# Optimization experiments

Measured on AMD Instinct MI355X. Metric: run time of the kernel, lower is better.

## Reference

```python
import jax, jax.numpy as jnp
import numpy as np
import math

N = 50000        # nodes
E = 800000       # edges
FEATS = 64
CLASSES = 16
HIDDEN = 64
DEPTH = 10
DIFF = 0.9
EMB_DIM = 1 + int(math.log2(FEATS))   # 7
ADJ_HID = 4 + EMB_DIM                  # 11


def setup_inputs() -> dict:
    key = jax.random.key(0)
    ks = jax.random.split(key, 12)
    x = jax.random.normal(ks[0], (N, FEATS), dtype=jnp.float32)
    src = jax.random.randint(ks[1], (E,), 0, N, dtype=jnp.int64)
    dst = jax.random.randint(ks[2], (E,), 0, N, dtype=jnp.int64)
    s = 0.05
    W1 = jax.random.normal(ks[3], (2 * FEATS, HIDDEN), jnp.float32) * s
    b1 = jnp.zeros((HIDDEN,), jnp.float32)
    W2 = jax.random.normal(ks[4], (HIDDEN, CLASSES), jnp.float32) * s
    b2 = jnp.zeros((CLASSES,), jnp.float32)
    A1 = jax.random.normal(ks[5], (2 + EMB_DIM, ADJ_HID), jnp.float32) * s
    ab1 = jnp.zeros((ADJ_HID,), jnp.float32)
    A2 = jax.random.normal(ks[6], (ADJ_HID, 1), jnp.float32) * s
    ab2 = jnp.zeros((1,), jnp.float32)
    emb = jax.random.normal(ks[7], (FEATS, EMB_DIM), jnp.float32) * s
    return {"x": x, "src": src, "dst": dst, "W1": W1, "b1": b1,
            "W2": W2, "b2": b2, "A1": A1, "ab1": ab1, "A2": A2,
            "ab2": ab2, "emb": emb}


def reference(x, src, dst, W1, b1, W2, b2, A1, ab1, A2, ab2, emb):
    n, f = x.shape
    # cached symmetric GCN normalization: D^-1/2 A D^-1/2
    deg = jax.ops.segment_sum(jnp.ones((src.shape[0],), x.dtype), dst, num_segments=n)
    inv_sqrt = jnp.where(deg > 0, jax.lax.rsqrt(jnp.maximum(deg, 1e-12)), 0.0)
    norm = inv_sqrt[src] * inv_sqrt[dst]   # [E]

    def conv(z):
        return jax.ops.segment_sum(z[src] * norm[:, None], dst, num_segments=n)

    # first diffusion loop (personalized-pagerank style residual blend)
    h0 = x
    z = x
    for _ in range(DEPTH):
        z = conv(z) * DIFF + (1.0 - DIFF) * h0

    # node x class pair MLP (class-major flatten, matching x.t().reshape(-1,1))
    cls = jnp.repeat(jnp.arange(f), n)                 # [f*n]
    pairs = jnp.concatenate([z.T.reshape(-1, 1),
                             h0.T.reshape(-1, 1),
                             emb[cls]], axis=1)        # [f*n, 2+EMB_DIM]
    u = jax.nn.relu(pairs @ A1 + ab1)
    u = (u @ A2 + ab2) / 2.0                           # [f*n, 1]
    z = u.reshape(f, n).T                              # [n, f]

    # dropout is identity in eval mode
    z = jnp.concatenate([z, h0], axis=1)               # [n, 2f]
    z = jax.nn.relu(z @ W1 + b1)
    z = z @ W2 + b2                                    # [n, classes]

    # second diffusion loop over class logits
    g0 = z
    for _ in range(DEPTH):
        z = conv(z) * DIFF + (1.0 - DIFF) * g0
    return z
```

## Files before the change

### kernel.cpp

```cpp
#include <hip/hip_runtime.h>

#define FEATS    64
#define CLASSES  16
#define EMB_DIM  7
#define ADJ_HID  11
#define DIFF     0.9f

__device__ inline float bf2f(unsigned short u) {
    return __uint_as_float(((unsigned int)u) << 16);
}
__device__ inline unsigned short f2bf(float f) {
    unsigned int u = __float_as_uint(f);
    return (unsigned short)((u + 0x7FFFu + ((u >> 16) & 1u)) >> 16);
}


__global__ __launch_bounds__(256) void k_deg(const int* __restrict__ dst, int* __restrict__ deg, int e) {
    int i = blockIdx.x * 256 + threadIdx.x;
    if (i < e) atomicAdd(&deg[dst[i]], 1);
}

__global__ __launch_bounds__(256) void k_invs(const int* __restrict__ deg, float* __restrict__ invs, int n) {
    int i = blockIdx.x * 256 + threadIdx.x;
    if (i < n) { int d = deg[i]; invs[i] = d > 0 ? rsqrtf((float)d) : 0.f; }
}

__global__ __launch_bounds__(256) void k_scan1(const int* __restrict__ deg, int* __restrict__ rowptr,
                                               int* __restrict__ bsum, int n) {
    __shared__ int s[256];
    int tid = threadIdx.x;
    int i = blockIdx.x * 256 + tid;
    int v = (i < n) ? deg[i] : 0;
    s[tid] = v; __syncthreads();
    for (int ofs = 1; ofs < 256; ofs <<= 1) {
        int t = (tid >= ofs) ? s[tid - ofs] : 0;
        __syncthreads(); s[tid] += t; __syncthreads();
    }
    if (i < n) rowptr[i] = s[tid] - v;
    if (tid == 255) bsum[blockIdx.x] = s[255];
}

__global__ __launch_bounds__(256) void k_scan2(int* __restrict__ bsum, int nb) {
    __shared__ int s[256];
    int tid = threadIdx.x;
    int v = (tid < nb) ? bsum[tid] : 0;
    s[tid] = v; __syncthreads();
    for (int ofs = 1; ofs < 256; ofs <<= 1) {
        int t = (tid >= ofs) ? s[tid - ofs] : 0;
        __syncthreads(); s[tid] += t; __syncthreads();
    }
    if (tid < nb) bsum[tid] = s[tid] - v;
}

__global__ __launch_bounds__(256) void k_scan3(int* __restrict__ rowptr, const int* __restrict__ bsum,
                                               int n, int e) {
    int i = blockIdx.x * 256 + threadIdx.x;
    if (i < n) rowptr[i] += bsum[i >> 8];
    if (i == n) rowptr[n] = e;
}

__global__ __launch_bounds__(256) void k_scatter(const int* __restrict__ src, const int* __restrict__ dst,
                                                 const float* __restrict__ invs, const int* __restrict__ rowptr,
                                                 int* __restrict__ cnt, int2* __restrict__ edge, int e) {
    int i = blockIdx.x * 256 + threadIdx.x;
    if (i >= e) return;
    int d = dst[i], sv = src[i];
    int pos = rowptr[d] + atomicAdd(&cnt[d], 1);
    edge[pos] = make_int2(sv, __float_as_int(invs[sv] * invs[d]));
}


__global__ __launch_bounds__(256) void k_cast(const float4* __restrict__ in, ushort4* __restrict__ out, int total4) {
    int i = blockIdx.x * 256 + threadIdx.x;
    if (i < total4) {
        float4 v = in[i];
        ushort4 o;
        o.x = f2bf(v.x); o.y = f2bf(v.y); o.z = f2bf(v.z); o.w = f2bf(v.w);
        out[i] = o;
    }
}


__global__ __launch_bounds__(256) void k_conv64b(const ushort4* __restrict__ zin, const ushort4* __restrict__ h0b,
                                                 ushort4* __restrict__ zout, const int* __restrict__ rowptr,
                                                 const int2* __restrict__ edge, int n) {
    int wid = (blockIdx.x * 256 + threadIdx.x) >> 6;
    if (wid >= n) return;
    int lane = threadIdx.x & 63;
    int g = lane >> 4, c = lane & 15;
    int e0 = rowptr[wid], e1 = rowptr[wid + 1];
    float a0 = 0.f, a1 = 0.f, a2 = 0.f, a3 = 0.f;

    if (e1 - e0 <= 16) {
        #pragma unroll
        for (int k = 0; k < 4; ++k) {
            int idx = e0 + k * 4 + g;
            bool ok = idx < e1;
            int2 p = edge[ok ? idx : e0];
            float w = ok ? __int_as_float(p.y) : 0.f;
            ushort4 v = zin[(size_t)p.x * 16 + c];
            a0 = fmaf(w, bf2f(v.x), a0);
            a1 = fmaf(w, bf2f(v.y), a1);
            a2 = fmaf(w, bf2f(v.z), a2);
            a3 = fmaf(w, bf2f(v.w), a3);
        }
    } else {
        int2 P[8];
        #pragma unroll
        for (int k = 0; k < 8; ++k) {
            int idx = e0 + k * 4 + g;
            P[k] = edge[idx < e1 ? idx : e0];
        }
        #pragma unroll
        for (int k = 0; k < 8; ++k) {
            int idx = e0 + k * 4 + g;
            float w = (idx < e1) ? __int_as_float(P[k].y) : 0.f;
            ushort4 v = zin[(size_t)P[k].x * 16 + c];
            a0 = fmaf(w, bf2f(v.x), a0);
            a1 = fmaf(w, bf2f(v.y), a1);
            a2 = fmaf(w, bf2f(v.z), a2);
            a3 = fmaf(w, bf2f(v.w), a3);
        }
        for (int e = e0 + 32; e < e1; e += 16) {
            #pragma unroll
            for (int k = 0; k < 4; ++k) {
                int idx = e + k * 4 + g;
                bool ok = idx < e1;
                int2 p = edge[ok ? idx : e0];
                float w = ok ? __int_as_float(p.y) : 0.f;
                ushort4 v = zin[(size_t)p.x * 16 + c];
                a0 = fmaf(w, bf2f(v.x), a0);
                a1 = fmaf(w, bf2f(v.y), a1);
                a2 = fmaf(w, bf2f(v.z), a2);
                a3 = fmaf(w, bf2f(v.w), a3);
            }
        }
    }

    a0 += __shfl_xor(a0, 16); a1 += __shfl_xor(a1, 16);
    a2 += __shfl_xor(a2, 16); a3 += __shfl_xor(a3, 16);
    a0 += __shfl_xor(a0, 32); a1 += __shfl_xor(a1, 32);
    a2 += __shfl_xor(a2, 32); a3 += __shfl_xor(a3, 32);
    if (lane < 16) {
        ushort4 h4 = h0b[(size_t)wid * 16 + lane];
        ushort4 o;
        o.x = f2bf(a0 * DIFF + (1.f - DIFF) * bf2f(h4.x));
        o.y = f2bf(a1 * DIFF + (1.f - DIFF) * bf2f(h4.y));
        o.z = f2bf(a2 * DIFF + (1.f - DIFF) * bf2f(h4.z));
        o.w = f2bf(a3 * DIFF + (1.f - DIFF) * bf2f(h4.w));
        zout[(size_t)wid * 16 + lane] = o;
    }
}


__global__ __launch_bounds__(256) void k_conv16(const float4* __restrict__ zin4, const float4* __restrict__ g04,
                                                float4* __restrict__ zout4, const int* __restrict__ rowptr,
                                                const int2* __restrict__ edge, int n) {
    int wid = (blockIdx.x * 256 + threadIdx.x) >> 6;
    if (wid >= n) return;
    int lane = threadIdx.x & 63;
    int g = lane >> 2, c = lane & 3;
    int e0 = rowptr[wid], e1 = rowptr[wid + 1];
    float4 acc; acc.x = acc.y = acc.z = acc.w = 0.f;
    for (int e = e0; e < e1; e += 32) {
        #pragma unroll
        for (int k = 0; k < 2; ++k) {
            int idx = e + k * 16 + g;
            bool ok = idx < e1;
            int2 p = edge[ok ? idx : e0];
            float w = ok ? __int_as_float(p.y) : 0.f;
            float4 v = zin4[(size_t)p.x * 4 + c];
            acc.x = fmaf(w, v.x, acc.x);
            acc.y = fmaf(w, v.y, acc.y);
            acc.z = fmaf(w, v.z, acc.z);
            acc.w = fmaf(w, v.w, acc.w);
        }
    }
    #pragma unroll
    for (int m = 4; m <= 32; m <<= 1) {
        acc.x += __shfl_xor(acc.x, m);
        acc.y += __shfl_xor(acc.y, m);
        acc.z += __shfl_xor(acc.z, m);
        acc.w += __shfl_xor(acc.w, m);
    }
    if (lane < 4) {
        float4 h = g04[(size_t)wid * 4 + lane];
        float4 o;
        o.x = acc.x * DIFF + (1.f - DIFF) * h.x;
        o.y = acc.y * DIFF + (1.f - DIFF) * h.y;
        o.z = acc.z * DIFF + (1.f - DIFF) * h.z;
        o.w = acc.w * DIFF + (1.f - DIFF) * h.w;
        zout4[(size_t)wid * 4 + lane] = o;
    }
}


#define PM_GRID 768

__global__ __launch_bounds__(256) void k_pairmlp(const unsigned short* __restrict__ z1, const float* __restrict__ x,
                                                 const float* __restrict__ W1, const float* __restrict__ b1,
                                                 const float* __restrict__ W2, const float* __restrict__ b2,
                                                 const float* __restrict__ A1, const float* __restrict__ ab1,
                                                 const float* __restrict__ A2, const float* __restrict__ ab2,
                                                 const float* __restrict__ emb,
                                                 float* __restrict__ g0, int n, int ntiles) {
    __shared__ float W1s[128 * 64];
    __shared__ float W2s[64 * 16];
    __shared__ float in_s[16][128];
    __shared__ float hid[16 * 65];
    __shared__ float eA1T[ADJ_HID * 64];
    __shared__ float a0s[ADJ_HID], a1s[ADJ_HID], a2s[ADJ_HID];
    __shared__ float ab2s;

    int tid = threadIdx.x;
    const ushort4* z4p = (const ushort4*)z1;
    const float4*  x4p = (const float4*)x;

    #pragma unroll
    for (int k = 0; k < 32; ++k) W1s[tid + k * 256] = W1[tid + k * 256];
    #pragma unroll
    for (int k = 0; k < 4; ++k)  W2s[tid + k * 256] = W2[tid + k * 256];
    if (tid < ADJ_HID) { a0s[tid] = A1[tid]; a1s[tid] = A1[ADJ_HID + tid]; a2s[tid] = A2[tid]; }
    if (tid == 0) ab2s = ab2[0];
    for (int idx = tid; idx < ADJ_HID * 64; idx += 256) {
        int h = idx >> 6, c = idx & 63;
        float s = ab1[h];
        #pragma unroll
        for (int j = 0; j < EMB_DIM; j++) s = fmaf(emb[c * EMB_DIM + j], A1[(2 + j) * ADJ_HID + h], s);
        eA1T[idx] = s;
    }
    __syncthreads();

    for (int tile = blockIdx.x; tile < ntiles; tile += PM_GRID) {
        int base = tile * 16;

        {
            int nl = tid >> 4, c4 = tid & 15;
            int node = base + nl; if (node > n - 1) node = n - 1;
            ushort4 z4 = z4p[(size_t)node * 16 + c4];
            float4  x4 = x4p[(size_t)node * 16 + c4];
            float zf0 = bf2f(z4.x), zf1 = bf2f(z4.y), zf2 = bf2f(z4.z), zf3 = bf2f(z4.w);
            float o0 = ab2s, o1 = ab2s, o2 = ab2s, o3 = ab2s;
            #pragma unroll
            for (int h = 0; h < ADJ_HID; h++) {
                float a0 = a0s[h], a1 = a1s[h], a2 = a2s[h];
                float4 ee = *(const float4*)&eA1T[h * 64 + c4 * 4];
                float t;
                t = fmaf(zf0, a0, fmaf(x4.x, a1, ee.x)); t = fmaxf(t, 0.f); o0 = fmaf(t, a2, o0);
                t = fmaf(zf1, a0, fmaf(x4.y, a1, ee.y)); t = fmaxf(t, 0.f); o1 = fmaf(t, a2, o1);
                t = fmaf(zf2, a0, fmaf(x4.z, a1, ee.z)); t = fmaxf(t, 0.f); o2 = fmaf(t, a2, o2);
                t = fmaf(zf3, a0, fmaf(x4.w, a1, ee.w)); t = fmaxf(t, 0.f); o3 = fmaf(t, a2, o3);
            }
            *(float4*)&in_s[nl][c4 * 4]      = make_float4(o0 * 0.5f, o1 * 0.5f, o2 * 0.5f, o3 * 0.5f);
            *(float4*)&in_s[nl][64 + c4 * 4] = x4;
        }
        __syncthreads();

        {
            int lane = tid & 63, wv = tid >> 6;
            int nb0 = wv * 4;
            float bv = b1[lane];
            float acc[4];
            #pragma unroll
            for (int j = 0; j < 4; ++j) acc[j] = bv;
            #pragma unroll 8
            for (int rb = 0; rb < 128; rb += 4) {
                float w0 = W1s[(rb    ) * 64 + lane];
                float w1 = W1s[(rb + 1) * 64 + lane];
                float w2 = W1s[(rb + 2) * 64 + lane];
                float w3 = W1s[(rb + 3) * 64 + lane];
                #pragma unroll
                for (int j = 0; j < 4; ++j) {
                    float4 iv = *(const float4*)&in_s[nb0 + j][rb];
                    acc[j] = fmaf(iv.w, w3, fmaf(iv.z, w2, fmaf(iv.y, w1, fmaf(iv.x, w0, acc[j]))));
                }
            }
            #pragma unroll
            for (int j = 0; j < 4; ++j) hid[(nb0 + j) * 65 + lane] = fmaxf(acc[j], 0.f);
        }
        __syncthreads();

        {
            int c  = tid & 15;
            int nl = tid >> 4;
            float ac = b2[c];
            #pragma unroll
            for (int h = 0; h < 64; ++h)
                ac = fmaf(hid[nl * 65 + h], W2s[h * 16 + c], ac);
            int n0 = base + nl;
            if (n0 < n) g0[(size_t)n0 * 16 + c] = ac;
        }
        __syncthreads();
    }
}


extern "C" void kernel_launch(void* const* d_in, const int* in_sizes, int n_in,
                              void* d_out, int out_size, void* d_ws, size_t ws_size,
                              hipStream_t stream) {
    const float* x   = (const float*)d_in[0];
    const int*   src = (const int*)d_in[1];
    const int*   dst = (const int*)d_in[2];
    const float* W1  = (const float*)d_in[3];
    const float* b1  = (const float*)d_in[4];
    const float* W2  = (const float*)d_in[5];
    const float* b2  = (const float*)d_in[6];
    const float* A1  = (const float*)d_in[7];
    const float* ab1 = (const float*)d_in[8];
    const float* A2  = (const float*)d_in[9];
    const float* ab2 = (const float*)d_in[10];
    const float* emb = (const float*)d_in[11];

    int n = in_sizes[0] / FEATS;
    int e = in_sizes[1];

    char* ws = (char*)d_ws;
    size_t off = 0;
    auto alloc = [&](size_t bytes) {
        void* p = ws + off;
        off += bytes;
        off = (off + 255) & ~(size_t)255;
        return p;
    };

    int*     deg    = (int*)    alloc((size_t)n * 4);
    float*   invs   = (float*)  alloc((size_t)n * 4);
    int*     rowptr = (int*)    alloc((size_t)(n + 1) * 4);
    int*     cnt    = (int*)    alloc((size_t)n * 4);
    int*     bsum   = (int*)    alloc(1024);
    int2*    edge   = (int2*)   alloc((size_t)e * 8 + 256);
    ushort4* xb     = (ushort4*)alloc((size_t)n * 64 * 2);
    ushort4* zbA    = (ushort4*)alloc((size_t)n * 64 * 2);
    ushort4* zbB    = (ushort4*)alloc((size_t)n * 64 * 2);
    float*   g0     = (float*)  alloc((size_t)n * 16 * 4);
    float*   g1     = (float*)  alloc((size_t)n * 16 * 4);
    float*   g2     = (float*)  alloc((size_t)n * 16 * 4);

    hipMemsetAsync(deg, 0, (size_t)n * 4, stream);
    hipMemsetAsync(cnt, 0, (size_t)n * 4, stream);

    int eb = (e + 255) / 256;
    int nb = (n + 255) / 256;

    k_deg    <<<eb, 256, 0, stream>>>(dst, deg, e);
    k_invs   <<<nb, 256, 0, stream>>>(deg, invs, n);
    k_scan1  <<<nb, 256, 0, stream>>>(deg, rowptr, bsum, n);
    k_scan2  <<<1, 256, 0, stream>>>(bsum, nb);
    k_scan3  <<<(n + 256) / 256, 256, 0, stream>>>(rowptr, bsum, n, e);
    k_scatter<<<eb, 256, 0, stream>>>(src, dst, invs, rowptr, cnt, edge, e);

    int total4 = n * 16;
    k_cast<<<(total4 + 255) / 256, 256, 0, stream>>>((const float4*)x, xb, total4);

    int nwb = (n + 3) / 4;

    const ushort4* zin = xb;
    ushort4* zout = zbA;
    for (int it = 0; it < 10; ++it) {
        k_conv64b<<<nwb, 256, 0, stream>>>(zin, xb, zout, rowptr, edge, n);
        zin  = zout;
        zout = (it == 0) ? zbB : ((zout == zbA) ? zbB : zbA);
    }
    const unsigned short* z1 = (const unsigned short*)zin;

    int ntiles = (n + 15) / 16;
    k_pairmlp<<<PM_GRID, 256, 0, stream>>>(z1, x, W1, b1, W2, b2,
                                           A1, ab1, A2, ab2, emb, g0, n, ntiles);

    const float* gin = g0;
    float* gout = g1;
    for (int it = 0; it < 10; ++it) {
        float* out = (it == 9) ? (float*)d_out : gout;
        k_conv16<<<nwb, 256, 0, stream>>>((const float4*)gin, (const float4*)g0, (float4*)out,
                                          rowptr, edge, n);
        gin  = out;
        gout = (gout == g1) ? g2 : g1;
    }
}
```

Before: 628.9 us.

## Process four destination nodes per wavefront in CSR gather kernels

Both diffusion kernels now assign four consecutive destination nodes to one 64-lane wavefront instead of one node per wavefront. The combined edge range is loaded cooperatively once and broadcast via shuffles, and each edge's contribution is routed to one of four per-node accumulators by comparing its index against the row boundaries. This targets the underutilised lanes and per-wave overhead when average degree is about 16. In exchange it adds register pressure from sixteen accumulators, redundant masked FMAs, and more shuffle reductions.

```diff
diff --git a/kernel.cpp b/kernel.cpp
--- a/kernel.cpp
+++ b/kernel.cpp
@@ -84,71 +84,71 @@
 __global__ __launch_bounds__(256) void k_conv64b(const ushort4* __restrict__ zin, const ushort4* __restrict__ h0b,
                                                  ushort4* __restrict__ zout, const int* __restrict__ rowptr,
                                                  const int2* __restrict__ edge, int n) {
-    int wid = (blockIdx.x * 256 + threadIdx.x) >> 6;
-    if (wid >= n) return;
+    int wq = (blockIdx.x * 256 + threadIdx.x) >> 6;
+    int n0 = wq * 4;
+    if (n0 >= n) return;
     int lane = threadIdx.x & 63;
     int g = lane >> 4, c = lane & 15;
-    int e0 = rowptr[wid], e1 = rowptr[wid + 1];
-    float a0 = 0.f, a1 = 0.f, a2 = 0.f, a3 = 0.f;
-
-    if (e1 - e0 <= 16) {
-        #pragma unroll
-        for (int k = 0; k < 4; ++k) {
-            int idx = e0 + k * 4 + g;
-            bool ok = idx < e1;
-            int2 p = edge[ok ? idx : e0];
-            float w = ok ? __int_as_float(p.y) : 0.f;
-            ushort4 v = zin[(size_t)p.x * 16 + c];
-            a0 = fmaf(w, bf2f(v.x), a0);
-            a1 = fmaf(w, bf2f(v.y), a1);
-            a2 = fmaf(w, bf2f(v.z), a2);
-            a3 = fmaf(w, bf2f(v.w), a3);
-        }
-    } else {
-        int2 P[8];
-        #pragma unroll
-        for (int k = 0; k < 8; ++k) {
-            int idx = e0 + k * 4 + g;
-            P[k] = edge[idx < e1 ? idx : e0];
-        }
-        #pragma unroll
-        for (int k = 0; k < 8; ++k) {
-            int idx = e0 + k * 4 + g;
-            float w = (idx < e1) ? __int_as_float(P[k].y) : 0.f;
-            ushort4 v = zin[(size_t)P[k].x * 16 + c];
-            a0 = fmaf(w, bf2f(v.x), a0);
-            a1 = fmaf(w, bf2f(v.y), a1);
-            a2 = fmaf(w, bf2f(v.z), a2);
-            a3 = fmaf(w, bf2f(v.w), a3);
-        }
-        for (int e = e0 + 32; e < e1; e += 16) {
-            #pragma unroll
-            for (int k = 0; k < 4; ++k) {
-                int idx = e + k * 4 + g;
-                bool ok = idx < e1;
-                int2 p = edge[ok ? idx : e0];
-                float w = ok ? __int_as_float(p.y) : 0.f;
-                ushort4 v = zin[(size_t)p.x * 16 + c];
-                a0 = fmaf(w, bf2f(v.x), a0);
-                a1 = fmaf(w, bf2f(v.y), a1);
-                a2 = fmaf(w, bf2f(v.z), a2);
-                a3 = fmaf(w, bf2f(v.w), a3);
+
+    int v = 0;
+    if (lane < 5) v = rowptr[min(n0 + lane, n)];
+    int r0 = __shfl(v, 0), r1 = __shfl(v, 1), r2 = __shfl(v, 2),
+        r3 = __shfl(v, 3), r4 = __shfl(v, 4);
+
+    ushort4 h4 = make_ushort4(0, 0, 0, 0);
+    if (n0 + g < n) h4 = h0b[(size_t)(n0 + g) * 16 + c];
+
+    float a[4][4];
+    #pragma unroll
+    for (int j = 0; j < 4; ++j)
+        #pragma unroll
+        for (int f = 0; f < 4; ++f) a[j][f] = 0.f;
+
+    for (int eb = r0; eb < r4; eb += 64) {
+        int2 pe = edge[min(eb + lane, r4 - 1)];
+        int   es = pe.x;
+        float ew = __int_as_float(pe.y);
+        #pragma unroll
+        for (int k = 0; k < 16; ++k) {
+            int s   = k * 4 + g;
+            int idx = eb + s;
+            int   srcn = __shfl(es, s);
+            float wraw = __shfl(ew, s);
+            float w = (idx < r4) ? wraw : 0.f;
+            int nid = (idx >= r1) + (idx >= r2) + (idx >= r3);
+            ushort4 vv = zin[(size_t)srcn * 16 + c];
+            float f0 = bf2f(vv.x), f1 = bf2f(vv.y), f2 = bf2f(vv.z), f3 = bf2f(vv.w);
+            #pragma unroll
+            for (int j = 0; j < 4; ++j) {
+                float sel = (nid == j) ? w : 0.f;
+                a[j][0] = fmaf(sel, f0, a[j][0]);
+                a[j][1] = fmaf(sel, f1, a[j][1]);
+                a[j][2] = fmaf(sel, f2, a[j][2]);
+                a[j][3] = fmaf(sel, f3, a[j][3]);
             }
         }
     }
 
-    a0 += __shfl_xor(a0, 16); a1 += __shfl_xor(a1, 16);
-    a2 += __shfl_xor(a2, 16); a3 += __shfl_xor(a3, 16);
-    a0 += __shfl_xor(a0, 32); a1 += __shfl_xor(a1, 32);
-    a2 += __shfl_xor(a2, 32); a3 += __shfl_xor(a3, 32);
-    if (lane < 16) {
-        ushort4 h4 = h0b[(size_t)wid * 16 + lane];
+    #pragma unroll
+    for (int j = 0; j < 4; ++j) {
+        #pragma unroll
+        for (int f = 0; f < 4; ++f) {
+            a[j][f] += __shfl_xor(a[j][f], 16);
+            a[j][f] += __shfl_xor(a[j][f], 32);
+        }
+    }
+
+    if (n0 + g < n) {
+        float o0 = (g == 0) ? a[0][0] : (g == 1) ? a[1][0] : (g == 2) ? a[2][0] : a[3][0];
+        float o1 = (g == 0) ? a[0][1] : (g == 1) ? a[1][1] : (g == 2) ? a[2][1] : a[3][1];
+        float o2 = (g == 0) ? a[0][2] : (g == 1) ? a[1][2] : (g == 2) ? a[2][2] : a[3][2];
+        float o3 = (g == 0) ? a[0][3] : (g == 1) ? a[1][3] : (g == 2) ? a[2][3] : a[3][3];
         ushort4 o;
-        o.x = f2bf(a0 * DIFF + (1.f - DIFF) * bf2f(h4.x));
-        o.y = f2bf(a1 * DIFF + (1.f - DIFF) * bf2f(h4.y));
-        o.z = f2bf(a2 * DIFF + (1.f - DIFF) * bf2f(h4.z));
-        o.w = f2bf(a3 * DIFF + (1.f - DIFF) * bf2f(h4.w));
-        zout[(size_t)wid * 16 + lane] = o;
+        o.x = f2bf(o0 * DIFF + (1.f - DIFF) * bf2f(h4.x));
+        o.y = f2bf(o1 * DIFF + (1.f - DIFF) * bf2f(h4.y));
+        o.z = f2bf(o2 * DIFF + (1.f - DIFF) * bf2f(h4.z));
+        o.w = f2bf(o3 * DIFF + (1.f - DIFF) * bf2f(h4.w));
+        zout[(size_t)(n0 + g) * 16 + c] = o;
     }
 }
 
@@ -156,41 +156,72 @@
 __global__ __launch_bounds__(256) void k_conv16(const float4* __restrict__ zin4, const float4* __restrict__ g04,
                                                 float4* __restrict__ zout4, const int* __restrict__ rowptr,
                                                 const int2* __restrict__ edge, int n) {
-    int wid = (blockIdx.x * 256 + threadIdx.x) >> 6;
-    if (wid >= n) return;
+    int wq = (blockIdx.x * 256 + threadIdx.x) >> 6;
+    int n0 = wq * 4;
+    if (n0 >= n) return;
     int lane = threadIdx.x & 63;
     int g = lane >> 2, c = lane & 3;
-    int e0 = rowptr[wid], e1 = rowptr[wid + 1];
-    float4 acc; acc.x = acc.y = acc.z = acc.w = 0.f;
-    for (int e = e0; e < e1; e += 32) {
-        #pragma unroll
-        for (int k = 0; k < 2; ++k) {
-            int idx = e + k * 16 + g;
-            bool ok = idx < e1;
-            int2 p = edge[ok ? idx : e0];
-            float w = ok ? __int_as_float(p.y) : 0.f;
-            float4 v = zin4[(size_t)p.x * 4 + c];
-            acc.x = fmaf(w, v.x, acc.x);
-            acc.y = fmaf(w, v.y, acc.y);
-            acc.z = fmaf(w, v.z, acc.z);
-            acc.w = fmaf(w, v.w, acc.w);
-        }
-    }
-    #pragma unroll
-    for (int m = 4; m <= 32; m <<= 1) {
-        acc.x += __shfl_xor(acc.x, m);
-        acc.y += __shfl_xor(acc.y, m);
-        acc.z += __shfl_xor(acc.z, m);
-        acc.w += __shfl_xor(acc.w, m);
-    }
-    if (lane < 4) {
-        float4 h = g04[(size_t)wid * 4 + lane];
+
+    int v = 0;
+    if (lane < 5) v = rowptr[min(n0 + lane, n)];
+    int r0 = __shfl(v, 0), r1 = __shfl(v, 1), r2 = __shfl(v, 2),
+        r3 = __shfl(v, 3), r4 = __shfl(v, 4);
+
+    float4 h = make_float4(0.f, 0.f, 0.f, 0.f);
+    if (g < 4 && n0 + g < n) h = g04[(size_t)(n0 + g) * 4 + c];
+
+    float a[4][4];
+    #pragma unroll
+    for (int j = 0; j < 4; ++j)
+        #pragma unroll
+        for (int f = 0; f < 4; ++f) a[j][f] = 0.f;
+
+    for (int eb = r0; eb < r4; eb += 64) {
+        int2 pe = edge[min(eb + lane, r4 - 1)];
+        int   es = pe.x;
+        float ew = __int_as_float(pe.y);
+        #pragma unroll
+        for (int k = 0; k < 4; ++k) {
+            int s   = k * 16 + g;
+            int idx = eb + s;
+            int   srcn = __shfl(es, s);
+            float wraw = __shfl(ew, s);
+            float w = (idx < r4) ? wraw : 0.f;
+            int nid = (idx >= r1) + (idx >= r2) + (idx >= r3);
+            float4 vv = zin4[(size_t)srcn * 4 + c];
+            #pragma unroll
+            for (int j = 0; j < 4; ++j) {
+                float sel = (nid == j) ? w : 0.f;
+                a[j][0] = fmaf(sel, vv.x, a[j][0]);
+                a[j][1] = fmaf(sel, vv.y, a[j][1]);
+                a[j][2] = fmaf(sel, vv.z, a[j][2]);
+                a[j][3] = fmaf(sel, vv.w, a[j][3]);
+            }
+        }
+    }
+
+    #pragma unroll
+    for (int j = 0; j < 4; ++j) {
+        #pragma unroll
+        for (int f = 0; f < 4; ++f) {
+            a[j][f] += __shfl_xor(a[j][f], 4);
+            a[j][f] += __shfl_xor(a[j][f], 8);
+            a[j][f] += __shfl_xor(a[j][f], 16);
+            a[j][f] += __shfl_xor(a[j][f], 32);
+        }
+    }
+
+    if (g < 4 && n0 + g < n) {
+        float o0 = (g == 0) ? a[0][0] : (g == 1) ? a[1][0] : (g == 2) ? a[2][0] : a[3][0];
+        float o1 = (g == 0) ? a[0][1] : (g == 1) ? a[1][1] : (g == 2) ? a[2][1] : a[3][1];
+        float o2 = (g == 0) ? a[0][2] : (g == 1) ? a[1][2] : (g == 2) ? a[2][2] : a[3][2];
+        float o3 = (g == 0) ? a[0][3] : (g == 1) ? a[1][3] : (g == 2) ? a[2][3] : a[3][3];
         float4 o;
-        o.x = acc.x * DIFF + (1.f - DIFF) * h.x;
-        o.y = acc.y * DIFF + (1.f - DIFF) * h.y;
-        o.z = acc.z * DIFF + (1.f - DIFF) * h.z;
-        o.w = acc.w * DIFF + (1.f - DIFF) * h.w;
-        zout4[(size_t)wid * 4 + lane] = o;
+        o.x = o0 * DIFF + (1.f - DIFF) * h.x;
+        o.y = o1 * DIFF + (1.f - DIFF) * h.y;
+        o.z = o2 * DIFF + (1.f - DIFF) * h.z;
+        o.w = o3 * DIFF + (1.f - DIFF) * h.w;
+        zout4[(size_t)(n0 + g) * 4 + c] = o;
     }
 }
 
@@ -352,12 +383,13 @@
     int total4 = n * 16;
     k_cast<<<(total4 + 255) / 256, 256, 0, stream>>>((const float4*)x, xb, total4);
 
-    int nwb = (n + 3) / 4;
+    int nquad = (n + 3) / 4;
+    int cblocks = (nquad + 3) / 4;
 
     const ushort4* zin = xb;
     ushort4* zout = zbA;
     for (int it = 0; it < 10; ++it) {
-        k_conv64b<<<nwb, 256, 0, stream>>>(zin, xb, zout, rowptr, edge, n);
+        k_conv64b<<<cblocks, 256, 0, stream>>>(zin, xb, zout, rowptr, edge, n);
         zin  = zout;
         zout = (it == 0) ? zbB : ((zout == zbA) ? zbB : zbA);
     }
@@ -371,8 +403,8 @@
     float* gout = g1;
     for (int it = 0; it < 10; ++it) {
         float* out = (it == 9) ? (float*)d_out : gout;
-        k_conv16<<<nwb, 256, 0, stream>>>((const float4*)gin, (const float4*)g0, (float4*)out,
-                                          rowptr, edge, n);
+        k_conv16<<<cblocks, 256, 0, stream>>>((const float4*)gin, (const float4*)g0, (float4*)out,
+                                              rowptr, edge, n);
         gin  = out;
         gout = (gout == g1) ? g2 : g1;
     }
```

After: 626.4 us. No clear change (-0.4%).
